# Kernel optimization log

Hardware: AMD Instinct MI355X
Metric: run time of the kernel (lower is better)

## Reference

```python
import jax, jax.numpy as jnp
import numpy as np

N, T = 128, 256
QN, QD = 16, 32           # Qn_num, Qn_dim
QL_SIZES = [100] * 8      # Ql category sizes
LD = 32                   # Ql_dim
H = 1024                  # hidden_dim
L = 2                     # layer_num
OUT = 2                   # output_dim
IN_DIM = QN * QD + len(QL_SIZES) * LD  # 768
EPS = 1e-5


def setup_inputs() -> dict:
    key = jax.random.key(0)
    ks = jax.random.split(key, 14)
    qn = jax.random.normal(ks[0], (N, T, QN), dtype=jnp.float32)
    ql = jax.random.randint(ks[1], (N, T, len(QL_SIZES)), 0, 100).astype(jnp.float32)
    x = jnp.concatenate([qn, ql], axis=2)  # [N,T,24]
    std = 1.0 / np.sqrt(H)
    u = lambda k, s: jax.random.uniform(k, s, minval=-std, maxval=std, dtype=jnp.float32)
    return dict(
        x=x,
        QnV=jax.random.normal(ks[2], (QN, QD), dtype=jnp.float32) * 0.5,
        QlV=jax.random.normal(ks[3], (sum(QL_SIZES), LD), dtype=jnp.float32) * 0.5,
        bn_gamma=jnp.ones((QN,), jnp.float32),
        bn_beta=jnp.zeros((QN,), jnp.float32),
        W0=u(ks[4], (IN_DIM + H, 4 * H)), b0=u(ks[5], (4 * H,)),
        W1=u(ks[6], (2 * H, 4 * H)), b1=u(ks[7], (4 * H,)),
        ln_gamma=u(ks[8], (L, 4, H)), ln_beta=u(ks[9], (L, 4, H)),
        fcW=u(ks[10], (H, OUT)), fcb=u(ks[11], (OUT,)),
    )


def _layernorm(v, g, b):
    m = v.mean(-1, keepdims=True)
    s = v.var(-1, keepdims=True)
    return (v - m) * jax.lax.rsqrt(s + EPS) * g + b


def reference(x, QnV, QlV, bn_gamma, bn_beta, W0, b0, W1, b1, ln_gamma, ln_beta, fcW, fcb):
    # ---- data_trans ----
    qn = x[:, :, :QN]                               # [N,T,QN] float features
    ql_idx = x[:, :, QN:].astype(jnp.int32)         # [N,T,Lq] category indices
    offsets = jnp.asarray(np.concatenate([[0], np.cumsum(QL_SIZES)[:-1]]), jnp.int32)
    ql_idx = ql_idx + offsets.reshape(1, 1, -1)
    # BatchNorm1d (training mode): stats over flattened N*T rows, per feature
    flat = qn.reshape(-1, QN)
    mu = flat.mean(0)
    var = flat.var(0)
    qn = (qn - mu) * jax.lax.rsqrt(var + EPS) * bn_gamma + bn_beta
    qn_emb = qn[..., None] * QnV                    # einsum ijk,kd->ijkd : [N,T,QN,QD]
    ql_emb = QlV[ql_idx]                            # [N,T,Lq,LD]
    feats = jnp.concatenate([qn_emb, ql_emb], axis=2).reshape(N, T, IN_DIM)

    Ws, bs = [W0, W1], [b0, b1]

    def step(carry, xt):  # xt: [N, IN_DIM]
        hn, cn = carry     # each [L, N, H]
        xcur = xt
        hs, cs = [], []
        for i in range(L):
            inp = jnp.concatenate([hn[i], xcur], axis=1)
            gates = inp @ Ws[i] + bs[i]             # [N, 4H]
            ig, fg, gg, og = jnp.split(gates, 4, axis=1)
            ig = jax.nn.sigmoid(_layernorm(ig, ln_gamma[i, 0], ln_beta[i, 0]))
            fg = jax.nn.sigmoid(_layernorm(fg, ln_gamma[i, 1], ln_beta[i, 1]))
            gn = _layernorm(gg, ln_gamma[i, 2], ln_beta[i, 2])
            og = jax.nn.sigmoid(_layernorm(og, ln_gamma[i, 3], ln_beta[i, 3]))
            c = cn[i] * fg + ig * jnp.tanh(gn)
            # NOTE: original adds the pre-tanh normalized cellgate (quirk, kept faithful)
            xcur = og * jnp.tanh(c) + gn
            hs.append(xcur)
            cs.append(c)
        return (jnp.stack(hs), jnp.stack(cs)), xcur  # emit last layer h

    h0 = jnp.zeros((L, N, H), jnp.float32)
    c0 = jnp.zeros((L, N, H), jnp.float32)
    xs = jnp.transpose(feats, (1, 0, 2))            # [T, N, IN_DIM]
    _, outs = jax.lax.scan(step, (h0, c0), xs)      # [T, N, H]
    outs = jnp.transpose(outs, (1, 0, 2))           # [N, T, H]
    logits = outs @ fcW + fcb                       # [N, T, OUT]
    return jax.nn.softmax(logits, axis=2)
```

## Files before the change

kernel.cpp:

```cpp
#include <hip/hip_runtime.h>
#include <math.h>


#define N_   128
#define T_   256
#define QN_  16
#define INX  24
#define H_   1024
#define G4   4096
#define FDIM 768
#define EPS_ 1e-5f
#define K0_  1792
#define K1_  2048
#define NSLOT 8
#define HSZ  ((size_t)N_ * H_)
#define SSLOT 16
#define SLSZ (512 * 8 * 16)

typedef unsigned short u16;
typedef unsigned int u32;
typedef unsigned long long u64;
typedef __attribute__((ext_vector_type(8))) short bf16x8;
typedef __attribute__((ext_vector_type(4))) float f32x4;

__device__ __forceinline__ float sigmoidf_(float v) { return 1.0f / (1.0f + expf(-v)); }

__device__ __forceinline__ u16 f2bf(float f) {
  unsigned u = __float_as_uint(f);
  u += 0x7fffu + ((u >> 16) & 1u);
  return (u16)(u >> 16);
}
__device__ __forceinline__ float bf2f(u16 x) {
  return __uint_as_float((u32)x << 16);
}

__device__ __forceinline__ void st_u64g(void* p, u64 v) {
  __hip_atomic_store((u64*)p, v, __ATOMIC_RELAXED, __HIP_MEMORY_SCOPE_AGENT);
}
__device__ __forceinline__ void st_f32g(float* p, float v) {
  __hip_atomic_store(p, v, __ATOMIC_RELAXED, __HIP_MEMORY_SCOPE_AGENT);
}
__device__ __forceinline__ void atomAdd_(float* p, float v) {
  __hip_atomic_fetch_add(p, v, __ATOMIC_RELAXED, __HIP_MEMORY_SCOPE_AGENT);
}

__global__ __launch_bounds__(256) void bn_stats_k(const float* __restrict__ x,
    const float* __restrict__ gamma, const float* __restrict__ beta,
    float* __restrict__ scale, float* __restrict__ shift) {
  int q = blockIdx.x;
  int tid = threadIdx.x;
  float s = 0.f, s2 = 0.f;
  for (int r = tid; r < N_ * T_; r += 256) {
    float v = x[(size_t)r * INX + q];
    s += v; s2 += v * v;
  }
  for (int off = 32; off; off >>= 1) { s += __shfl_down(s, off); s2 += __shfl_down(s2, off); }
  __shared__ float red[2][4];
  int w = tid >> 6;
  if ((tid & 63) == 0) { red[0][w] = s; red[1][w] = s2; }
  __syncthreads();
  if (tid == 0) {
    float S = 0.f, S2 = 0.f;
    for (int i = 0; i < 4; ++i) { S += red[0][i]; S2 += red[1][i]; }
    float m   = S  / (float)(N_ * T_);
    float var = S2 / (float)(N_ * T_) - m * m;
    float rs  = rsqrtf(var + EPS_);
    scale[q] = rs * gamma[q];
    shift[q] = beta[q] - m * rs * gamma[q];
  }
}

__global__ __launch_bounds__(256) void feats_all_k(const float* __restrict__ x,
    const float* __restrict__ scale, const float* __restrict__ shift,
    const float* __restrict__ QnV, const float* __restrict__ QlV,
    u16* __restrict__ ft) {
  int rid = blockIdx.x;
  int t = rid >> 7, n = rid & 127;
  const float* xr = x + ((size_t)n * T_ + t) * INX;
  u16* frow = ft + (size_t)rid * FDIM;
  for (int f = threadIdx.x; f < FDIM; f += 256) {
    int d = f & 31;
    float v;
    if (f < 512) {
      int q = f >> 5;
      v = (xr[q] * scale[q] + shift[q]) * QnV[q * 32 + d];
    } else {
      int cg_ = (f - 512) >> 5;
      int idx = (int)xr[QN_ + cg_] + cg_ * 100;
      v = QlV[idx * 32 + d];
    }
    frow[f] = f2bf(v);
  }
}

__global__ __launch_bounds__(256) void wconv_k(const float* __restrict__ W,
                                               u16* __restrict__ WtP, int K) {
  __shared__ u16 L[64][72];
  int tid = threadIdx.x;
  int k0 = blockIdx.x * 64, n0 = blockIdx.y * 64;
#pragma unroll
  for (int it = 0; it < 16; ++it) {
    int e = it * 256 + tid;
    int r = e >> 6, c = e & 63;
    L[r][c] = f2bf(W[(size_t)(k0 + r) * G4 + n0 + c]);
  }
  __syncthreads();
  int n = tid >> 2, ks = (tid & 3) << 4;
  int col = n0 + n;
  int b = (col & 1023) >> 3;
  int j = (col >> 10) * 8 + (col & 7);
  u16* dst = WtP + ((size_t)(b * 32 + j)) * K + k0 + ks;
#pragma unroll
  for (int jj = 0; jj < 16; ++jj) dst[jj] = L[ks + jj][n];
}

#define SUBC(fam, sub)  cnts[((fam) * 8 + (sub)) * 16]
#define FLAGR(fam, rep) cnts[(32 + (fam) * 32 + (rep)) * 16]

__device__ __forceinline__ void arrive_(u32* cnts, int fam, int sub) {
  __hip_atomic_fetch_add(&SUBC(fam, sub), 1u,
                         __ATOMIC_RELAXED, __HIP_MEMORY_SCOPE_AGENT);
}
__device__ __forceinline__ void pollsub_(u32* cnts, int fam, int sub, u32 tgt16) {
  while (__hip_atomic_load(&SUBC(fam, sub), __ATOMIC_RELAXED, __HIP_MEMORY_SCOPE_AGENT) < tgt16)
    __builtin_amdgcn_s_sleep(1);
}
__device__ __forceinline__ void pollflag_(u32* cnts, int fam, int rep, u32 t1) {
  while (__hip_atomic_load(&FLAGR(fam, rep), __ATOMIC_RELAXED, __HIP_MEMORY_SCOPE_AGENT) < t1)
    __builtin_amdgcn_s_sleep(1);
}
__device__ __forceinline__ void acqf_(int tid) {
  if (tid < 64) __builtin_amdgcn_fence(__ATOMIC_ACQUIRE, "agent");
  __syncthreads();
}

__device__ __forceinline__ void waitfam_(u32* cnts, int fam, u32 t1, int isCloser,
                                         int tid, int rep, int bpFam, u32 bpT1) {
  if (isCloser) { if (tid < 8) pollsub_(cnts, fam, tid, t1 * 16u); }
  else          { if (tid == 0) pollflag_(cnts, fam, rep, t1); }
  if (tid == 8 && bpFam >= 0) pollflag_(cnts, bpFam, rep, bpT1);
  __syncthreads();
  if (isCloser && tid < 32)
    __hip_atomic_store(&FLAGR(fam, tid), t1, __ATOMIC_RELAXED, __HIP_MEMORY_SCOPE_AGENT);
}

template<int NS>
__device__ __forceinline__ void gpart(f32x4& a0, f32x4& a1,
    const u16* __restrict__ abase, const u16* __restrict__ wb0,
    const u16* __restrict__ wb1, int cb, int swz, int g) {
#pragma unroll 8
  for (int kc = 0; kc < NS; ++kc) {
    bf16x8 av = *(const bf16x8*)(abase + kc * 32);
    int c = ((cb + kc * 4 + g) ^ swz) << 3;
    bf16x8 bv0 = *(const bf16x8*)(wb0 + c);
    bf16x8 bv1 = *(const bf16x8*)(wb1 + c);
    a0 = __builtin_amdgcn_mfma_f32_16x16x32_bf16(av, bv0, a0, 0, 0, 0);
    a1 = __builtin_amdgcn_mfma_f32_16x16x32_bf16(av, bv1, a1, 0, 0, 0);
  }
}

__device__ __forceinline__ float lnrm2(float v, float2 sq, float g_, float b_) {
  float mean = sq.x * (1.f / (float)H_);
  float var  = sq.y * (1.f / (float)H_) - mean * mean;
  return (v - mean) * rsqrtf(var + EPS_) * g_ + b_;
}

__global__ __launch_bounds__(512, 2) void persist_k(
    const u16* __restrict__ WtP0, const u16* __restrict__ WtP1,
    const u16* __restrict__ ft,
    u16* __restrict__ h0s, u16* __restrict__ h1s,
    const float* __restrict__ b0, const float* __restrict__ b1,
    const float* __restrict__ lng, const float* __restrict__ lnb,
    const float* __restrict__ fcW, const float* __restrict__ fcb,
    float* __restrict__ statsA, float* __restrict__ statsB,
    u32* __restrict__ cnts, float* __restrict__ out) {
  __shared__ u16 wlds[32 * K1_];
  __shared__ float2 sstat[512];
  const int bcu = blockIdx.x, tid = threadIdx.x;
  const int isL0 = bcu < 128;
  const int b    = isL0 ? bcu : bcu - 128;
  const int wave = tid >> 6, lane = tid & 63;
  const int vcol = lane & 15, g4 = lane >> 4;
  const int ga = vcol >> 3, hh = vcol & 7;
  const int swz = vcol & 7;
  const int rowA  = wave * 16 + vcol;
  const int wbase = wave * 16;
  const int sub   = b >> 4;
  const int bank  = b & 7;
  const int rep   = b & 31;
  const int fph   = b & 7;
  const int hbase = b * 8;
  const int K = isL0 ? K0_ : K1_;

  {
    const u16* wsrc = isL0 ? WtP0 + (size_t)b * 32 * K0_
                           : WtP1 + (size_t)b * 32 * K1_;
    int kc8 = K >> 3;
    for (int cid = tid; cid < 32 * kc8; cid += 512) {
      int j = cid / kc8, ck = cid - j * kc8;
      *(bf16x8*)&wlds[j * K + ((ck ^ (j & 7)) << 3)] =
          *(const bf16x8*)&wsrc[(size_t)j * K + (ck << 3)];
    }
  }
  __syncthreads();
  acqf_(tid);

  const u16* wb0p = &wlds[vcol * K];
  const u16* wb1p = &wlds[(vcol + 16) * K];

  const float* bW   = isL0 ? b0 : b1;
  const float* lngW = isL0 ? lng : lng + 4 * H_;
  const float* lnbW = isL0 ? lnb : lnb + 4 * H_;
  const int colA = ga * H_ + hbase + hh;
  const int colB = (ga + 2) * H_ + hbase + hh;
  const float bias0v = bW[colA], bias1v = bW[colB];
  const float lng0v = lngW[colA], lnb0v = lnbW[colA];
  const float lng1v = lngW[colB], lnb1v = lnbW[colB];
  const float fcb0 = fcb[0], fcb1 = fcb[1];

  float cst[4] = {0.f, 0.f, 0.f, 0.f};

  if (isL0) {
    f32x4 acN0 = {0.f, 0.f, 0.f, 0.f}, acN1 = acN0;
    gpart<24>(acN0, acN1, ft + (size_t)rowA * FDIM + g4 * 8, wb0p, wb1p, 128, swz, g4);

    for (int t = 0; t < T_; ++t) {
      const u32 t1 = (u32)(t + 1);
      u16* h0w = h0s + (size_t)(t & (NSLOT - 1)) * HSZ;
      const u16* h0r = h0s + (size_t)((t - 1) & (NSLOT - 1)) * HSZ;
      float* stA = statsA + (size_t)(t & (SSLOT - 1)) * SLSZ;

      f32x4 ac0 = acN0, ac1 = acN1;
      gpart<32>(ac0, ac1, h0r + (size_t)rowA * H_ + g4 * 8, wb0p, wb1p, 0, swz, g4);
      f32x4 accb0, accb1;
#pragma unroll
      for (int r = 0; r < 4; ++r) { accb0[r] = ac0[r] + bias0v; accb1[r] = ac1[r] + bias1v; }

#pragma unroll
      for (int r = 0; r < 4; ++r) {
        int row = wbase + g4 * 4 + r;
        float s0 = accb0[r], q0 = s0 * s0, s1 = accb1[r], q1 = s1 * s1;
#pragma unroll
        for (int off = 1; off <= 4; off <<= 1) {
          s0 += __shfl_xor(s0, off); q0 += __shfl_xor(q0, off);
          s1 += __shfl_xor(s1, off); q1 += __shfl_xor(q1, off);
        }
        if (hh == 0) {
          float* l0 = &stA[(((row * 4 + ga) * 8) + bank) * 16];
          float* l1 = &stA[(((row * 4 + ga + 2) * 8) + bank) * 16];
          atomAdd_(l0, s0);     atomAdd_(l0 + 1, q0);
          atomAdd_(l1, s1);     atomAdd_(l1 + 1, q1);
        }
      }
      asm volatile("s_waitcnt vmcnt(0)" ::: "memory");
      __syncthreads();
      if (tid == 0) arrive_(cnts, 0, sub);

      {
        float* zs = statsA + (size_t)((t + 8) & (SSLOT - 1)) * SLSZ;
        if (tid < 64) st_f32g(&zs[(b * 32 + (tid >> 1)) * 16 + (tid & 1)], 0.f);
        int tn = (t + 1 < T_) ? t + 1 : t;
        acN0[0] = 0.f; acN0[1] = 0.f; acN0[2] = 0.f; acN0[3] = 0.f;
        acN1 = acN0;
        gpart<24>(acN0, acN1, ft + ((size_t)tn * N_ + rowA) * FDIM + g4 * 8,
                  wb0p, wb1p, 128, swz, g4);
      }
      waitfam_(cnts, 0, t1, b == 0, tid, rep,
               (t >= 7) ? 2 : -1, (u32)(t - 6));

      {
        const float* lp = &stA[(size_t)tid * 128];
        float s = 0.f, q = 0.f;
#pragma unroll
        for (int k = 0; k < 8; ++k) {
          float2 v = *(const float2*)(lp + k * 16);
          s += v.x; q += v.y;
        }
        sstat[tid] = make_float2(s, q);
      }
      __syncthreads();

#pragma unroll
      for (int r = 0; r < 4; ++r) {
        int row = wbase + g4 * 4 + r;
        float2 sv0 = sstat[row * 4 + ga];
        float2 sv1 = sstat[row * 4 + ga + 2];
        float nv0 = lnrm2(accb0[r], sv0, lng0v, lnb0v);
        float nv1 = lnrm2(accb1[r], sv1, lng1v, lnb1v);
        float o0 = __shfl_xor(nv0, 8), o1 = __shfl_xor(nv1, 8);
        float vi = ga ? o0 : nv0;
        float vf = ga ? nv0 : o0;
        float vg = ga ? o1 : nv1;
        float vo = ga ? nv1 : o1;
        float igt = sigmoidf_(vi), fgt = sigmoidf_(vf), ogt = sigmoidf_(vo);
        float cn = cst[r] * fgt + igt * tanhf(vg);
        float xn = ogt * tanhf(cn) + vg;
        cst[r] = cn;
        u32 xv = f2bf(xn);
        u32 oth = __shfl_xor((int)xv, 1);
        u32 pr = (hh & 1) ? ((oth & 0xffffu) | (xv << 16)) : ((xv & 0xffffu) | (oth << 16));
        u32 p2 = __shfl_xor((int)pr, 2);
        if (ga == 0 && (hh & 3) == 0)
          st_u64g(&h0w[(size_t)row * H_ + hbase + hh], ((u64)p2 << 32) | pr);
      }
      asm volatile("s_waitcnt vmcnt(0)" ::: "memory");
      __syncthreads();
      if (tid == 0) arrive_(cnts, 1, sub);
      waitfam_(cnts, 1, t1, b == 1, tid, rep, -1, 0);
      if ((t & 7) == fph) acqf_(tid);
    }
  } else {
    for (int t = 0; t < T_; ++t) {
      const u32 t1 = (u32)(t + 1);
      const u16* h0r = h0s + (size_t)(t & (NSLOT - 1)) * HSZ;
      u16* h1w = h1s + (size_t)(t & (NSLOT - 1)) * HSZ;
      const u16* h1r = h1s + (size_t)((t - 1) & (NSLOT - 1)) * HSZ;
      float* stA = statsB + (size_t)(t & (SSLOT - 1)) * SLSZ;

      f32x4 ac0 = {0.f, 0.f, 0.f, 0.f}, ac1 = ac0;
      gpart<32>(ac0, ac1, h1r + (size_t)rowA * H_ + g4 * 8, wb0p, wb1p, 0, swz, g4);

      if (tid == 0) pollflag_(cnts, 1, rep, t1);
      __syncthreads();
      gpart<32>(ac0, ac1, h0r + (size_t)rowA * H_ + g4 * 8, wb0p, wb1p, 128, swz, g4);
      f32x4 accb0, accb1;
#pragma unroll
      for (int r = 0; r < 4; ++r) { accb0[r] = ac0[r] + bias0v; accb1[r] = ac1[r] + bias1v; }

#pragma unroll
      for (int r = 0; r < 4; ++r) {
        int row = wbase + g4 * 4 + r;
        float s0 = accb0[r], q0 = s0 * s0, s1 = accb1[r], q1 = s1 * s1;
#pragma unroll
        for (int off = 1; off <= 4; off <<= 1) {
          s0 += __shfl_xor(s0, off); q0 += __shfl_xor(q0, off);
          s1 += __shfl_xor(s1, off); q1 += __shfl_xor(q1, off);
        }
        if (hh == 0) {
          float* l0 = &stA[(((row * 4 + ga) * 8) + bank) * 16];
          float* l1 = &stA[(((row * 4 + ga + 2) * 8) + bank) * 16];
          atomAdd_(l0, s0);     atomAdd_(l0 + 1, q0);
          atomAdd_(l1, s1);     atomAdd_(l1 + 1, q1);
        }
      }
      asm volatile("s_waitcnt vmcnt(0)" ::: "memory");
      __syncthreads();
      if (tid == 0) arrive_(cnts, 2, sub);

      if (t > 0 && wave == 0) {
        const u16* hrow = h1r + (size_t)b * H_;
        int col = lane * 16;
        bf16x8 v0 = *(const bf16x8*)(hrow + col);
        bf16x8 v1 = *(const bf16x8*)(hrow + col + 8);
        float L0v = 0.f, L1v = 0.f;
#pragma unroll
        for (int j = 0; j < 8; ++j) {
          float x0 = bf2f((u16)v0[j]);
          float2 fw = *(const float2*)&fcW[(col + j) * 2];
          L0v = fmaf(x0, fw.x, L0v); L1v = fmaf(x0, fw.y, L1v);
          float x1 = bf2f((u16)v1[j]);
          float2 fw2 = *(const float2*)&fcW[(col + 8 + j) * 2];
          L0v = fmaf(x1, fw2.x, L0v); L1v = fmaf(x1, fw2.y, L1v);
        }
#pragma unroll
        for (int off = 1; off <= 32; off <<= 1) { L0v += __shfl_xor(L0v, off); L1v += __shfl_xor(L1v, off); }
        if (lane == 0) {
          L0v += fcb0; L1v += fcb1;
          float mx = fmaxf(L0v, L1v);
          float e0 = expf(L0v - mx), e1 = expf(L1v - mx);
          float inv = 1.f / (e0 + e1);
          *(float2*)&out[((size_t)b * T_ + (t - 1)) * 2] = make_float2(e0 * inv, e1 * inv);
        }
      }
      {
        float* zs = statsB + (size_t)((t + 8) & (SSLOT - 1)) * SLSZ;
        if (tid >= 64 && tid < 128)
          st_f32g(&zs[(b * 32 + ((tid - 64) >> 1)) * 16 + (tid & 1)], 0.f);
      }
      waitfam_(cnts, 2, t1, b == 0, tid, rep, -1, 0);

      {
        const float* lp = &stA[(size_t)tid * 128];
        float s = 0.f, q = 0.f;
#pragma unroll
        for (int k = 0; k < 8; ++k) {
          float2 v = *(const float2*)(lp + k * 16);
          s += v.x; q += v.y;
        }
        sstat[tid] = make_float2(s, q);
      }
      __syncthreads();

#pragma unroll
      for (int r = 0; r < 4; ++r) {
        int row = wbase + g4 * 4 + r;
        float2 sv0 = sstat[row * 4 + ga];
        float2 sv1 = sstat[row * 4 + ga + 2];
        float nv0 = lnrm2(accb0[r], sv0, lng0v, lnb0v);
        float nv1 = lnrm2(accb1[r], sv1, lng1v, lnb1v);
        float o0 = __shfl_xor(nv0, 8), o1 = __shfl_xor(nv1, 8);
        float vi = ga ? o0 : nv0;
        float vf = ga ? nv0 : o0;
        float vg = ga ? o1 : nv1;
        float vo = ga ? nv1 : o1;
        float igt = sigmoidf_(vi), fgt = sigmoidf_(vf), ogt = sigmoidf_(vo);
        float cn = cst[r] * fgt + igt * tanhf(vg);
        float xn = ogt * tanhf(cn) + vg;
        cst[r] = cn;
        u32 xv = f2bf(xn);
        u32 oth = __shfl_xor((int)xv, 1);
        u32 pr = (hh & 1) ? ((oth & 0xffffu) | (xv << 16)) : ((xv & 0xffffu) | (oth << 16));
        u32 p2 = __shfl_xor((int)pr, 2);
        if (ga == 0 && (hh & 3) == 0)
          st_u64g(&h1w[(size_t)row * H_ + hbase + hh], ((u64)p2 << 32) | pr);
      }
      asm volatile("s_waitcnt vmcnt(0)" ::: "memory");
      __syncthreads();
      if (tid == 0) arrive_(cnts, 3, sub);
      waitfam_(cnts, 3, t1, b == 1, tid, rep, -1, 0);
      if ((t & 7) == fph) acqf_(tid);
    }
    if (wave == 0) {
      const u16* hrow = h1s + (size_t)((T_ - 1) & (NSLOT - 1)) * HSZ + (size_t)b * H_;
      int col = lane * 16;
      bf16x8 v0 = *(const bf16x8*)(hrow + col);
      bf16x8 v1 = *(const bf16x8*)(hrow + col + 8);
      float L0v = 0.f, L1v = 0.f;
#pragma unroll
      for (int j = 0; j < 8; ++j) {
        float x0 = bf2f((u16)v0[j]);
        float2 fw = *(const float2*)&fcW[(col + j) * 2];
        L0v = fmaf(x0, fw.x, L0v); L1v = fmaf(x0, fw.y, L1v);
        float x1 = bf2f((u16)v1[j]);
        float2 fw2 = *(const float2*)&fcW[(col + 8 + j) * 2];
        L0v = fmaf(x1, fw2.x, L0v); L1v = fmaf(x1, fw2.y, L1v);
      }
#pragma unroll
      for (int off = 1; off <= 32; off <<= 1) { L0v += __shfl_xor(L0v, off); L1v += __shfl_xor(L1v, off); }
      if (lane == 0) {
        L0v += fcb0; L1v += fcb1;
        float mx = fmaxf(L0v, L1v);
        float e0 = expf(L0v - mx), e1 = expf(L1v - mx);
        float inv = 1.f / (e0 + e1);
        *(float2*)&out[((size_t)b * T_ + (T_ - 1)) * 2] = make_float2(e0 * inv, e1 * inv);
      }
    }
  }
}

extern "C" void kernel_launch(void* const* d_in, const int* in_sizes, int n_in,
                              void* d_out, int out_size, void* d_ws, size_t ws_size,
                              hipStream_t stream) {
  const float* x   = (const float*)d_in[0];
  const float* QnV = (const float*)d_in[1];
  const float* QlV = (const float*)d_in[2];
  const float* bng = (const float*)d_in[3];
  const float* bnb = (const float*)d_in[4];
  const float* W0  = (const float*)d_in[5];
  const float* b0  = (const float*)d_in[6];
  const float* W1  = (const float*)d_in[7];
  const float* b1  = (const float*)d_in[8];
  const float* lng = (const float*)d_in[9];
  const float* lnb = (const float*)d_in[10];
  const float* fcW = (const float*)d_in[11];
  const float* fcb = (const float*)d_in[12];
  float* out = (float*)d_out;

  u32*   cnts   = (u32*)d_ws;
  float* statsA = (float*)(cnts + 4096);
  float* statsB = statsA + (size_t)SSLOT * SLSZ;
  u16*   h0s    = (u16*)(statsB + (size_t)SSLOT * SLSZ);
  u16*   h1s    = h0s + (size_t)NSLOT * HSZ;
  size_t zero_bytes = (size_t)((char*)(h1s + (size_t)NSLOT * HSZ) - (char*)d_ws);

  float* scale = (float*)(h1s + (size_t)NSLOT * HSZ);
  float* shift = scale + 64;
  u16* ft   = (u16*)(shift + 64);
  u16* WtP0 = ft + (size_t)N_ * T_ * FDIM;
  u16* WtP1 = WtP0 + (size_t)G4 * K0_;

  hipMemsetAsync(d_ws, 0, zero_bytes, stream);

  bn_stats_k<<<QN_, 256, 0, stream>>>(x, bng, bnb, scale, shift);
  feats_all_k<<<N_ * T_, 256, 0, stream>>>(x, scale, shift, QnV, QlV, ft);
  wconv_k<<<dim3(K0_ / 64, G4 / 64), 256, 0, stream>>>(W0, WtP0, K0_);
  wconv_k<<<dim3(K1_ / 64, G4 / 64), 256, 0, stream>>>(W1, WtP1, K1_);

  void* args[] = {
    (void*)&WtP0, (void*)&WtP1, (void*)&ft, (void*)&h0s, (void*)&h1s,
    (void*)&b0, (void*)&b1, (void*)&lng, (void*)&lnb,
    (void*)&fcW, (void*)&fcb, (void*)&statsA, (void*)&statsB,
    (void*)&cnts, (void*)&out
  };
  hipLaunchCooperativeKernel((void*)persist_k, dim3(256), dim3(512), args, 0, stream);
}
```

Measured before the change: 8.310 ms.

## Replace stats barrier with per-slot arrival counters polled by consumers

```diff
diff --git a/kernel.cpp b/kernel.cpp
--- a/kernel.cpp
+++ b/kernel.cpp
@@ -40,7 +40,16 @@
 __device__ __forceinline__ void st_f32g(float* p, float v) {
   __hip_atomic_store(p, v, __ATOMIC_RELAXED, __HIP_MEMORY_SCOPE_AGENT);
 }
+__device__ __forceinline__ u64 ld_u64g(const void* p) {
+  return __hip_atomic_load((const u64*)p, __ATOMIC_RELAXED, __HIP_MEMORY_SCOPE_AGENT);
+}
+__device__ __forceinline__ u32 ld_u32g(const u32* p) {
+  return __hip_atomic_load(p, __ATOMIC_RELAXED, __HIP_MEMORY_SCOPE_AGENT);
+}
 __device__ __forceinline__ void atomAdd_(float* p, float v) {
+  __hip_atomic_fetch_add(p, v, __ATOMIC_RELAXED, __HIP_MEMORY_SCOPE_AGENT);
+}
+__device__ __forceinline__ void atomAddU_(u32* p, u32 v) {
   __hip_atomic_fetch_add(p, v, __ATOMIC_RELAXED, __HIP_MEMORY_SCOPE_AGENT);
 }
 
@@ -163,6 +172,49 @@
   float mean = sq.x * (1.f / (float)H_);
   float var  = sq.y * (1.f / (float)H_) - mean * mean;
   return (v - mean) * rsqrtf(var + EPS_) * g_ + b_;
+}
+
+__device__ __forceinline__ void stats_publish(float* stA, const f32x4& accb0,
+    const f32x4& accb1, int wbase, int g4, int ga, int hh, int bank) {
+#pragma unroll
+  for (int r = 0; r < 4; ++r) {
+    int row = wbase + g4 * 4 + r;
+    float s0 = accb0[r], q0 = s0 * s0, s1 = accb1[r], q1 = s1 * s1;
+#pragma unroll
+    for (int off = 1; off <= 4; off <<= 1) {
+      s0 += __shfl_xor(s0, off); q0 += __shfl_xor(q0, off);
+      s1 += __shfl_xor(s1, off); q1 += __shfl_xor(q1, off);
+    }
+    if (hh == 0) {
+      float* l0 = &stA[(((row * 4 + ga) * 8) + bank) * 16];
+      float* l1 = &stA[(((row * 4 + ga + 2) * 8) + bank) * 16];
+      atomAdd_(l0 + 2, s0);  atomAdd_(l0 + 3, q0);
+      atomAdd_(l1 + 2, s1);  atomAdd_(l1 + 3, q1);
+    }
+  }
+  asm volatile("s_waitcnt vmcnt(0)" ::: "memory");
+#pragma unroll
+  for (int r = 0; r < 4; ++r) {
+    int row = wbase + g4 * 4 + r;
+    if (hh == 0) {
+      atomAddU_((u32*)&stA[(((row * 4 + ga) * 8) + bank) * 16], 1u);
+      atomAddU_((u32*)&stA[(((row * 4 + ga + 2) * 8) + bank) * 16], 1u);
+    }
+  }
+}
+
+__device__ __forceinline__ float2 stats_gather(const float* stA, int tid) {
+  const float* lp = stA + (size_t)tid * 128;
+  float s = 0.f, q = 0.f;
+#pragma unroll
+  for (int k = 0; k < 8; ++k) {
+    const u32* ln = (const u32*)(lp + k * 16);
+    while (ld_u32g(ln) < 16u) __builtin_amdgcn_s_sleep(1);
+    u64 v = ld_u64g(lp + k * 16 + 2);
+    s += __uint_as_float((u32)v);
+    q += __uint_as_float((u32)(v >> 32));
+  }
+  return make_float2(s, q);
 }
 
 __global__ __launch_bounds__(512, 2) void persist_k(
@@ -236,48 +288,19 @@
 #pragma unroll
       for (int r = 0; r < 4; ++r) { accb0[r] = ac0[r] + bias0v; accb1[r] = ac1[r] + bias1v; }
 
-#pragma unroll
-      for (int r = 0; r < 4; ++r) {
-        int row = wbase + g4 * 4 + r;
-        float s0 = accb0[r], q0 = s0 * s0, s1 = accb1[r], q1 = s1 * s1;
-#pragma unroll
-        for (int off = 1; off <= 4; off <<= 1) {
-          s0 += __shfl_xor(s0, off); q0 += __shfl_xor(q0, off);
-          s1 += __shfl_xor(s1, off); q1 += __shfl_xor(q1, off);
-        }
-        if (hh == 0) {
-          float* l0 = &stA[(((row * 4 + ga) * 8) + bank) * 16];
-          float* l1 = &stA[(((row * 4 + ga + 2) * 8) + bank) * 16];
-          atomAdd_(l0, s0);     atomAdd_(l0 + 1, q0);
-          atomAdd_(l1, s1);     atomAdd_(l1 + 1, q1);
-        }
-      }
-      asm volatile("s_waitcnt vmcnt(0)" ::: "memory");
-      __syncthreads();
-      if (tid == 0) arrive_(cnts, 0, sub);
+      stats_publish(stA, accb0, accb1, wbase, g4, ga, hh, bank);
 
       {
         float* zs = statsA + (size_t)((t + 8) & (SSLOT - 1)) * SLSZ;
-        if (tid < 64) st_f32g(&zs[(b * 32 + (tid >> 1)) * 16 + (tid & 1)], 0.f);
+        if (tid < 128) st_f32g(&zs[(b * 32 + (tid >> 2)) * 16 + (tid & 3)], 0.f);
         int tn = (t + 1 < T_) ? t + 1 : t;
         acN0[0] = 0.f; acN0[1] = 0.f; acN0[2] = 0.f; acN0[3] = 0.f;
         acN1 = acN0;
         gpart<24>(acN0, acN1, ft + ((size_t)tn * N_ + rowA) * FDIM + g4 * 8,
                   wb0p, wb1p, 128, swz, g4);
       }
-      waitfam_(cnts, 0, t1, b == 0, tid, rep,
-               (t >= 7) ? 2 : -1, (u32)(t - 6));
-
-      {
-        const float* lp = &stA[(size_t)tid * 128];
-        float s = 0.f, q = 0.f;
-#pragma unroll
-        for (int k = 0; k < 8; ++k) {
-          float2 v = *(const float2*)(lp + k * 16);
-          s += v.x; q += v.y;
-        }
-        sstat[tid] = make_float2(s, q);
-      }
+
+      sstat[tid] = stats_gather(stA, tid);
       __syncthreads();
 
 #pragma unroll
@@ -306,7 +329,8 @@
       asm volatile("s_waitcnt vmcnt(0)" ::: "memory");
       __syncthreads();
       if (tid == 0) arrive_(cnts, 1, sub);
-      waitfam_(cnts, 1, t1, b == 1, tid, rep, -1, 0);
+      waitfam_(cnts, 1, t1, b == 1, tid, rep,
+               (t >= 7) ? 3 : -1, (t1 >= 8) ? t1 - 7 : 0);
       if ((t & 7) == fph) acqf_(tid);
     }
   } else {
@@ -327,25 +351,7 @@
 #pragma unroll
       for (int r = 0; r < 4; ++r) { accb0[r] = ac0[r] + bias0v; accb1[r] = ac1[r] + bias1v; }
 
-#pragma unroll
-      for (int r = 0; r < 4; ++r) {
-        int row = wbase + g4 * 4 + r;
-        float s0 = accb0[r], q0 = s0 * s0, s1 = accb1[r], q1 = s1 * s1;
-#pragma unroll
-        for (int off = 1; off <= 4; off <<= 1) {
-          s0 += __shfl_xor(s0, off); q0 += __shfl_xor(q0, off);
-          s1 += __shfl_xor(s1, off); q1 += __shfl_xor(q1, off);
-        }
-        if (hh == 0) {
-          float* l0 = &stA[(((row * 4 + ga) * 8) + bank) * 16];
-          float* l1 = &stA[(((row * 4 + ga + 2) * 8) + bank) * 16];
-          atomAdd_(l0, s0);     atomAdd_(l0 + 1, q0);
-          atomAdd_(l1, s1);     atomAdd_(l1 + 1, q1);
-        }
-      }
-      asm volatile("s_waitcnt vmcnt(0)" ::: "memory");
-      __syncthreads();
-      if (tid == 0) arrive_(cnts, 2, sub);
+      stats_publish(stA, accb0, accb1, wbase, g4, ga, hh, bank);
 
       if (t > 0 && wave == 0) {
         const u16* hrow = h1r + (size_t)b * H_;
@@ -374,21 +380,11 @@
       }
       {
         float* zs = statsB + (size_t)((t + 8) & (SSLOT - 1)) * SLSZ;
-        if (tid >= 64 && tid < 128)
-          st_f32g(&zs[(b * 32 + ((tid - 64) >> 1)) * 16 + (tid & 1)], 0.f);
-      }
-      waitfam_(cnts, 2, t1, b == 0, tid, rep, -1, 0);
-
-      {
-        const float* lp = &stA[(size_t)tid * 128];
-        float s = 0.f, q = 0.f;
-#pragma unroll
-        for (int k = 0; k < 8; ++k) {
-          float2 v = *(const float2*)(lp + k * 16);
-          s += v.x; q += v.y;
-        }
-        sstat[tid] = make_float2(s, q);
-      }
+        if (tid >= 128 && tid < 256)
+          st_f32g(&zs[(b * 32 + ((tid - 128) >> 2)) * 16 + (tid & 3)], 0.f);
+      }
+
+      sstat[tid] = stats_gather(stA, tid);
       __syncthreads();
 
 #pragma unroll
```

Measured after the change: 13.45 ms. +61.8%, slower.
